# Kernel optimization log

Measured on AMD Instinct MI355X. Metric: run time of the kernel, lower is better.

## Reference

```python
import jax, jax.numpy as jnp
import numpy as np

ALPHA, BETA, INIT_P = 100.0, 1000.0, 2.0
K_NEIGHBORS = 24


def index_points(pts, idx):
    # pts: [B,N,C], idx: [B,...] int -> [B,...,C]
    B = pts.shape[0]
    b = jnp.arange(B).reshape((B,) + (1,) * (idx.ndim - 1))
    return pts[b, idx]


def fps(xyz, m):
    # furthest point sampling, deterministic start at index 0. xyz: [B,N,3]
    B, N, _ = xyz.shape
    def step(carry, _):
        dist, far = carry
        centroid = xyz[jnp.arange(B), far]              # [B,3]
        d = jnp.sum((xyz - centroid[:, None, :]) ** 2, -1)
        dist = jnp.minimum(dist, d)
        nxt = jnp.argmax(dist, -1).astype(jnp.int32)
        return (dist, nxt), far
    init = (jnp.full((B, N), 1e10, xyz.dtype), jnp.zeros((B,), jnp.int32))
    _, idx = jax.lax.scan(step, init, None, length=m)
    return idx.T                                        # [B,m]


def knn_indices(k, xyz, centers):
    # squared distances [B,G,N], k smallest
    d = (jnp.sum(centers ** 2, -1)[..., None]
         - 2.0 * jnp.einsum('bgc,bnc->bgn', centers, xyz)
         + jnp.sum(xyz ** 2, -1)[:, None, :])
    _, idx = jax.lax.top_k(-d, k)
    return idx                                          # [B,G,K]


def normalize(x, ref):
    # torch: mean = ref.unsqueeze(-2); std over ALL elements of (x-mean), ddof=1
    d = x - ref[..., None, :]
    std = jnp.std(d, ddof=1)
    return d / (std + 1e-5)


def fourier_map(t, Bmat):
    # t: [B,7,G,K]; Bmat: [7, C//2] (already includes scale) -> [B,C,G,K]
    x = jnp.transpose(t, (0, 2, 3, 1))                  # [B,G,K,7]
    proj = 2.0 * jnp.pi * (x @ Bmat)                    # [B,G,K,C/2]
    f = jnp.concatenate([jnp.sin(proj), jnp.cos(proj)], -1)
    f = jnp.sign(f) * jnp.abs(f) ** 5
    return jnp.transpose(f, (0, 3, 1, 2))


def tr_embed(my_dim, t):
    # t: [B,3,G,K] -> [B,my_dim,G,K]
    B, C, G, K = t.shape
    F = my_dim // (2 * C)
    dim_embed = ALPHA ** (jnp.arange(F, dtype=t.dtype) / F)
    div = BETA * t[..., None] / dim_embed               # [B,3,G,K,F]
    pe = jnp.stack([jnp.sin(div), jnp.cos(div)], -1).reshape(B, C, G, K, 2 * F)
    pe = jnp.transpose(pe, (0, 1, 4, 2, 3)).reshape(B, my_dim, G, K)
    return pe


def lga(lc_xyz, lc_x, knn_xyz, knn_x, Bmat):
    B, G, K, C = knn_x.shape
    knn_x = normalize(knn_x, lc_x)
    knn_xyz = normalize(knn_xyz, lc_xyz)
    lc_rep = jnp.transpose(jnp.broadcast_to(lc_xyz[:, :, None, :], (B, G, K, 3)), (0, 3, 1, 2))
    knn_xyz_t = jnp.transpose(knn_xyz, (0, 3, 1, 2))    # [B,3,G,K]
    knn_x_t = jnp.transpose(knn_x, (0, 3, 1, 2))        # [B,C,G,K]
    cross = jnp.cross(knn_xyz_t, lc_rep, axis=1)
    dot = jnp.sum(knn_xyz_t * lc_rep, 1, keepdims=True)
    emb_in = jnp.concatenate([knn_xyz_t, cross, dot], 1)  # [B,7,G,K]
    emb = fourier_map(emb_in, Bmat)                       # [B,C,G,K]
    knn_x_w = jnp.concatenate([knn_x_t, emb], 1)          # [B,2C,G,K]
    pe = tr_embed(2 * C, knn_xyz_t) + tr_embed(2 * C, lc_rep)
    return (knn_x_w + pe) * pe


def k_anp(x):
    # x: [B,2C,G,K], data-dependent p-norm attention over K
    std = jnp.std(x, axis=-1, ddof=1, keepdims=True)
    p = jax.lax.stop_gradient(INIT_P + jnp.log1p(std.mean()))  # torch uses .item()
    norm = jnp.sum(jnp.abs(x) ** p, -1, keepdims=True) ** (1.0 / p)
    lc = norm / (norm + 1e-8)
    e = jnp.exp(lc)
    return (x * e).mean(-1) / e.mean(-1)                # [B,2C,G]


def bn_gelu(x, gamma, beta):
    # BatchNorm1d in training mode (batch stats, biased var) + exact GELU
    mean = x.mean((0, 2), keepdims=True)
    var = ((x - mean) ** 2).mean((0, 2), keepdims=True)
    y = (x - mean) / jnp.sqrt(var + 1e-5) * gamma[None, :, None] + beta[None, :, None]
    return jax.nn.gelu(y, approximate=False)


def stage(xyz, x, group_num, Bmat, gamma, beta):
    # xyz: [B,N,3]; x: [B,C,N]
    feats = jnp.transpose(x, (0, 2, 1))
    fi = fps(xyz, group_num)
    lc_xyz = index_points(xyz, fi)
    lc_x = index_points(feats, fi)
    ki = knn_indices(K_NEIGHBORS, xyz, lc_xyz)
    knn_xyz = index_points(xyz, ki)
    knn_x = index_points(feats, ki)
    w = lga(lc_xyz, lc_x, knn_xyz, knn_x, Bmat)
    pooled = k_anp(w) + w.mean(-1)                      # [B,2C,G]
    return lc_xyz, bn_gelu(pooled, gamma, beta)


def setup_inputs() -> dict:
    key = jax.random.key(0)
    k1, k2, k3, k4 = jax.random.split(key, 4)
    B, N, C0 = 4, 4096, 72
    return {
        'xyz': jax.random.uniform(k1, (B, N, 3), jnp.float32),
        'x': jax.random.normal(k2, (B, C0, N), jnp.float32),
        'fourier_B0': jax.random.normal(k3, (7, C0 // 2), jnp.float32) * 50.0,
        'fourier_B1': jax.random.normal(k4, (7, C0), jnp.float32) * 50.0,
        'bn_gamma0': jnp.ones((2 * C0,), jnp.float32),
        'bn_beta0': jnp.zeros((2 * C0,), jnp.float32),
        'bn_gamma1': jnp.ones((4 * C0,), jnp.float32),
        'bn_beta1': jnp.zeros((4 * C0,), jnp.float32),
    }


def reference(xyz, x, fourier_B0, fourier_B1, bn_gamma0, bn_beta0, bn_gamma1, bn_beta1):
    N = xyz.shape[1]
    xyz, x = stage(xyz, x, N // 2, fourier_B0, bn_gamma0, bn_beta0)   # -> [B,144,2048]
    xyz, x = stage(xyz, x, N // 4, fourier_B1, bn_gamma1, bn_beta1)   # -> [B,288,1024]
    return x
```

## Files before the change

kernel.cpp:

```cpp
#include <hip/hip_runtime.h>
#include <math.h>

#define KNB 24

typedef float v2f __attribute__((ext_vector_type(2)));

__global__ void k_transpose(const float* __restrict__ x, float* __restrict__ feats,
                            int B, int C, int N) {
    int idx = blockIdx.x * blockDim.x + threadIdx.x;
    int tot = B * C * N;
    if (idx >= tot) return;
    int n = idx % N; int t = idx / N; int c = t % C; int b = t / C;
    feats[((size_t)b * N + n) * C + c] = x[idx];
}

template<int CTRL>
__device__ __forceinline__ float dppmax(float v) {
    int t = __builtin_amdgcn_update_dpp(0, __float_as_int(v), CTRL, 0xf, 0xf, true);
    return fmaxf(v, __int_as_float(t));
}
template<int CTRL>
__device__ __forceinline__ unsigned dppmaxu(unsigned v) {
    unsigned t = (unsigned)__builtin_amdgcn_update_dpp(0, (int)v, CTRL, 0xf, 0xf, true);
    return v > t ? v : t;
}

template<int NPT, int NWAVE>
__global__ __launch_bounds__(64 * NWAVE) void k_fps_t(const float* __restrict__ xyz,
                                                      int* __restrict__ fi,
                                                      int N, int M) {
#pragma clang fp contract(off)
    const int NP2 = NPT / 2;
    const int b = blockIdx.x;
    const int tid = threadIdx.x;
    const int lane = tid & 63;
    const int wid = tid >> 6;
    extern __shared__ char smc[];
    unsigned long long* keys = (unsigned long long*)smc;
    int* fi_lds = (int*)(smc + 2 * NWAVE * 8);
    size_t poff = ((size_t)(2 * NWAVE * 8) + (size_t)M * 4 + 15) & ~(size_t)15;
    float4* pts = (float4*)(smc + poff);

    const float* p = xyz + (size_t)b * N * 3;
    for (int i = tid; i < N; i += 64 * NWAVE)
        pts[i] = make_float4(p[i*3], p[i*3+1], p[i*3+2], 0.0f);
    __syncthreads();

    const int base = tid * NPT;
    v2f rx[NP2], ry[NP2], rz[NP2], dist[NP2];
#pragma unroll
    for (int j = 0; j < NP2; ++j) {
        float4 a = pts[base + 2*j];
        float4 c = pts[base + 2*j + 1];
        rx[j] = (v2f){a.x, c.x}; ry[j] = (v2f){a.y, c.y}; rz[j] = (v2f){a.z, c.z};
        dist[j] = (v2f){1e10f, 1e10f};
    }

    int far = 0;
    float4 cpt = pts[0];
    float cx = cpt.x, cy = cpt.y, cz = cpt.z;
    for (int it = 0; it < M; ++it) {
        if (tid == 0) fi_lds[it] = far;
        v2f cx2 = (v2f){cx, cx}, cy2 = (v2f){cy, cy}, cz2 = (v2f){cz, cz};
        v2f bv2 = (v2f){-1.0f, -1.0f};
#pragma unroll
        for (int j = 0; j < NP2; ++j) {
            v2f dx = rx[j] - cx2, dy = ry[j] - cy2, dz = rz[j] - cz2;
            v2f d = (dx*dx + dy*dy) + dz*dz;
            v2f dd = __builtin_elementwise_min(dist[j], d);
            dist[j] = dd;
            bv2 = __builtin_elementwise_max(bv2, dd);
        }
        float bv = fmaxf(bv2.x, bv2.y);
        int bi = 0;
#pragma unroll
        for (int j = NP2 - 1; j >= 0; --j) {
            if (dist[j].y == bv) bi = base + 2*j + 1;
            if (dist[j].x == bv) bi = base + 2*j;
        }
        float r = bv;
        r = dppmax<0x111>(r); r = dppmax<0x112>(r);
        r = dppmax<0x114>(r); r = dppmax<0x118>(r);
        r = dppmax<0x142>(r); r = dppmax<0x143>(r);
        float wmax = __int_as_float(__builtin_amdgcn_readlane(__float_as_int(r), 63));
        unsigned long long mask = __ballot(bv == wmax);
        int src = __builtin_ctzll(mask);
        int wbi = __builtin_amdgcn_readlane(bi, src);
        unsigned long long key =
            ((unsigned long long)__float_as_uint(wmax) << 32) | (unsigned)(~wbi);
        if (lane == 0) keys[(it & 1) * NWAVE + wid] = key;
        __syncthreads();
        unsigned long long k0 = keys[(it & 1) * NWAVE + 0];
#pragma unroll
        for (int w = 1; w < NWAVE; ++w) {
            unsigned long long kw = keys[(it & 1) * NWAVE + w];
            if (kw > k0) k0 = kw;
        }
        far = (int)(~(unsigned)k0);
        float4 c = pts[far];
        cx = c.x; cy = c.y; cz = c.z;
    }
    __syncthreads();
    for (int i = tid; i < M; i += 64 * NWAVE) fi[b * M + i] = fi_lds[i];
}

template<int NPT>
__global__ __launch_bounds__(256) void k_knn_t(const float* __restrict__ xyz,
                                               const float* __restrict__ feats,
                                               const int* __restrict__ fi,
                                               float* __restrict__ lc_xyz,
                                               float* __restrict__ lc_x,
                                               int* __restrict__ ki,
                                               double* __restrict__ part,
                                               int B, int N, int G, int C, int identity) {
#pragma clang fp contract(off)
    int bg = blockIdx.x; int b = bg / G; int g = bg % G;
    int idx = identity ? g : fi[bg];
    const int tid = threadIdx.x;
    const int lane = tid & 63;
    const int wid = tid >> 6;
    __shared__ unsigned long long keys[2][4];
    __shared__ int kis[KNB];
    __shared__ float cfeat[144];
    const float* p = xyz + (size_t)b * N * 3;
    float cx = p[idx*3], cy = p[idx*3+1], cz = p[idx*3+2];
    if (tid < 3) lc_xyz[(size_t)bg * 3 + tid] = p[idx*3 + tid];
    for (int c = tid; c < C; c += 256) {
        float v = feats[((size_t)b * N + idx) * C + c];
        lc_x[(size_t)bg * C + c] = v;
        cfeat[c] = v;
    }
    float cc = (cx*cx + cy*cy) + cz*cz;
    const int base = tid * NPT;
    float dist[NPT];
#pragma unroll
    for (int j = 0; j < NPT; ++j) {
        float x0 = p[(base+j)*3], x1 = p[(base+j)*3+1], x2 = p[(base+j)*3+2];
        float xx = (x0*x0 + x1*x1) + x2*x2;
        float dt = (cx*x0 + cy*x1) + cz*x2;
        dist[j] = (cc - 2.0f*dt) + xx;
    }
    for (int kk = 0; kk < KNB; ++kk) {
        float bv = 1e30f;
#pragma unroll
        for (int j = 0; j < NPT; ++j) bv = fminf(bv, dist[j]);
        int lj = 0;
#pragma unroll
        for (int j = NPT - 1; j >= 0; --j) if (dist[j] == bv) lj = j;
        unsigned ub = ~__float_as_uint(bv);
        unsigned r = ub;
        r = dppmaxu<0x111>(r); r = dppmaxu<0x112>(r);
        r = dppmaxu<0x114>(r); r = dppmaxu<0x118>(r);
        r = dppmaxu<0x142>(r); r = dppmaxu<0x143>(r);
        unsigned uwin = (unsigned)__builtin_amdgcn_readlane((int)r, 63);
        unsigned long long mask = __ballot(ub == uwin);
        int src = __builtin_ctzll(mask);
        int gi = __builtin_amdgcn_readlane(base + lj, src);
        unsigned long long key = ((unsigned long long)uwin << 32) | (unsigned)(~gi);
        if (lane == 0) keys[kk & 1][wid] = key;
        __syncthreads();
        unsigned long long k0 = keys[kk & 1][0];
#pragma unroll
        for (int w = 1; w < 4; ++w) {
            unsigned long long kw = keys[kk & 1][w];
            if (kw > k0) k0 = kw;
        }
        int win = (int)(~(unsigned)k0);
        if (tid == 0) kis[kk] = win;
        if (win >= base && win < base + NPT) {
            int wj = win - base;
#pragma unroll
            for (int j = 0; j < NPT; ++j) if (j == wj) dist[j] = 1e30f;
        }
    }
    __syncthreads();
    if (tid < KNB) ki[(size_t)bg * KNB + tid] = kis[tid];
    double s = 0.0, s2 = 0.0, s3 = 0.0, s4 = 0.0;
    for (int i = tid; i < KNB * C; i += 256) {
        int k = i / C, c = i - k * C;
        float d = feats[((size_t)b * N + kis[k]) * C + c] - cfeat[c];
        s += (double)d; s2 += (double)d * (double)d;
    }
    if (tid < KNB * 3) {
        int k = tid / 3, c = tid - k * 3;
        float ctr = (c == 0) ? cx : ((c == 1) ? cy : cz);
        float d = p[kis[k] * 3 + c] - ctr;
        s3 += (double)d; s4 += (double)d * (double)d;
    }
    for (int off = 32; off > 0; off >>= 1) {
        s += __shfl_down(s, off); s2 += __shfl_down(s2, off);
        s3 += __shfl_down(s3, off); s4 += __shfl_down(s4, off);
    }
    __shared__ double sw[4][4];
    if ((tid & 63) == 0) {
        sw[wid][0] = s; sw[wid][1] = s2; sw[wid][2] = s3; sw[wid][3] = s4;
    }
    __syncthreads();
    if (tid == 0) {
        double t0 = 0.0, t1 = 0.0, t2 = 0.0, t3 = 0.0;
        for (int w = 0; w < 4; ++w) {
            t0 += sw[w][0]; t1 += sw[w][1]; t2 += sw[w][2]; t3 += sw[w][3];
        }
        double* q = part + (size_t)bg * 4;
        q[0] = t0; q[1] = t1; q[2] = t2; q[3] = t3;
    }
}

__global__ __launch_bounds__(1024) void k_reduce(const double* __restrict__ part,
                                                 double* __restrict__ acc, int n) {
    double s0 = 0.0, s1 = 0.0, s2 = 0.0, s3 = 0.0;
    for (int i = threadIdx.x; i < n; i += 1024) {
        const double* q = part + (size_t)i * 4;
        s0 += q[0]; s1 += q[1]; s2 += q[2]; s3 += q[3];
    }
    for (int off = 32; off > 0; off >>= 1) {
        s0 += __shfl_down(s0, off); s1 += __shfl_down(s1, off);
        s2 += __shfl_down(s2, off); s3 += __shfl_down(s3, off);
    }
    __shared__ double sw[16][4];
    int wid = threadIdx.x >> 6;
    if ((threadIdx.x & 63) == 0) {
        sw[wid][0] = s0; sw[wid][1] = s1; sw[wid][2] = s2; sw[wid][3] = s3;
    }
    __syncthreads();
    if (threadIdx.x == 0) {
        double t0 = 0.0, t1 = 0.0, t2 = 0.0, t3 = 0.0;
        for (int w = 0; w < 16; ++w) {
            t0 += sw[w][0]; t1 += sw[w][1]; t2 += sw[w][2]; t3 += sw[w][3];
        }
        acc[0] = t0; acc[1] = t1; acc[2] = t2; acc[3] = t3;
    }
}

__global__ __launch_bounds__(256) void k_feature(
    const float* __restrict__ xyz, const float* __restrict__ feats,
    const float* __restrict__ lc_xyz, const float* __restrict__ lc_x,
    const int* __restrict__ ki, const float* __restrict__ Bmat,
    const double* __restrict__ accp, float* __restrict__ pooled,
    int B, int N, int G, int C, double nx, double nz)
{
    int bg = blockIdx.x; int b = bg / G; int g = bg % G;
    int tid = threadIdx.x;
    int C2 = C >> 1;
    int Cout = 2 * C;
    int F = C / 3;
    extern __shared__ float sm[];
    float* t7    = sm;
    float* sxyzn = t7 + KNB * 7;
    int*   kidx  = (int*)(sxyzn + KNB * 3);
    float* semb  = (float*)(kidx + KNB);
    float* sfeat = semb + KNB * C;

    double a0 = accp[0], a1 = accp[1], a2 = accp[2], a3 = accp[3];
    double vx = (a1 - a0 * a0 / nx) / (nx - 1.0);
    float invx = 1.0f / (sqrtf((float)vx) + 1e-5f);
    double vz = (a3 - a2 * a2 / nz) / (nz - 1.0);
    float invz = 1.0f / (sqrtf((float)vz) + 1e-5f);

    float l0 = lc_xyz[(size_t)bg*3], l1 = lc_xyz[(size_t)bg*3+1], l2 = lc_xyz[(size_t)bg*3+2];

    if (tid < KNB) {
        int idx = ki[(size_t)bg * KNB + tid];
        kidx[tid] = idx;
        const float* q = xyz + ((size_t)b * N + idx) * 3;
        float a0f = (q[0]-l0)*invz, a1f = (q[1]-l1)*invz, a2f = (q[2]-l2)*invz;
        float c0 = a1f*l2 - a2f*l1;
        float c1 = a2f*l0 - a0f*l2;
        float c2 = a0f*l1 - a1f*l0;
        float dt = (a0f*l0 + a1f*l1) + a2f*l2;
        float* tp = t7 + tid * 7;
        tp[0]=a0f; tp[1]=a1f; tp[2]=a2f; tp[3]=c0; tp[4]=c1; tp[5]=c2; tp[6]=dt;
        sxyzn[tid*3]=a0f; sxyzn[tid*3+1]=a1f; sxyzn[tid*3+2]=a2f;
    }
    __syncthreads();
    for (int i = tid; i < KNB * C; i += blockDim.x) {
        int k = i / C, c = i - k * C;
        sfeat[i] = feats[((size_t)b * N + kidx[k]) * C + c];
    }
    const float TWO_PI = 6.2831854820251465f;
    for (int i = tid; i < KNB * C2; i += blockDim.x) {
        int k = i / C2, m2 = i % C2;
        const float* tp = t7 + k * 7;
        float s = 0.0f;
        for (int j = 0; j < 7; ++j) s += tp[j] * Bmat[j * C2 + m2];
        float pr = TWO_PI * s;
        float sn, cs;
        __sincosf(pr, &sn, &cs);
        float sn2 = sn*sn, cs2 = cs*cs;
        semb[k*C + m2]      = sn2*sn2*sn;
        semb[k*C + C2 + m2] = cs2*cs2*cs;
    }
    __syncthreads();
    for (int m = tid; m < Cout; m += blockDim.x) {
        int c3 = m / (2 * F);
        int r  = m % (2 * F);
        int f  = r >> 1;
        int trig = r & 1;
        float de = __powf(100.0f, (float)f / (float)F);
        float rde = 1000.0f / de;
        float lv = (c3 == 0) ? l0 : ((c3 == 1) ? l1 : l2);
        float a2v = lv * rde;
        float pe2 = trig ? __cosf(a2v) : __sinf(a2v);
        float lfm = (m < C) ? lc_x[(size_t)bg * C + m] : 0.0f;
        float acc = 0.0f;
        for (int k = 0; k < KNB; ++k) {
            float v;
            if (m < C) {
                v = (sfeat[k * C + m] - lfm) * invx;
            } else {
                v = semb[k * C + (m - C)];
            }
            float a1v = sxyzn[k*3 + c3] * rde;
            float pe1 = trig ? __cosf(a1v) : __sinf(a1v);
            float pe = pe1 + pe2;
            acc += (v + pe) * pe;
        }
        float mean = acc / 24.0f;
        pooled[((size_t)b * Cout + m) * G + g] = 2.0f * mean;
    }
}

__global__ __launch_bounds__(256) void k_bn(const float* __restrict__ pooled,
                                            const float* __restrict__ gamma,
                                            const float* __restrict__ beta,
                                            float* __restrict__ out,
                                            int B, int Cout, int G, int transposed) {
    int m = blockIdx.x;
    double s = 0.0, s2 = 0.0;
    for (int i = threadIdx.x; i < B * G; i += 256) {
        int b = i / G, g = i % G;
        float v = pooled[((size_t)b * Cout + m) * G + g];
        s += (double)v; s2 += (double)v * (double)v;
    }
    for (int off = 32; off > 0; off >>= 1) { s += __shfl_down(s, off); s2 += __shfl_down(s2, off); }
    __shared__ double sw[4], sw2[4];
    __shared__ float smv[2];
    int wid = threadIdx.x >> 6;
    if ((threadIdx.x & 63) == 0) { sw[wid] = s; sw2[wid] = s2; }
    __syncthreads();
    if (threadIdx.x == 0) {
        double ts = sw[0] + sw[1] + sw[2] + sw[3];
        double ts2 = sw2[0] + sw2[1] + sw2[2] + sw2[3];
        double n = (double)(B * G);
        double mean = ts / n;
        double var = ts2 / n - mean * mean;
        smv[0] = (float)mean; smv[1] = (float)var;
    }
    __syncthreads();
    float mean = smv[0], var = smv[1];
    float ga = gamma[m], be = beta[m];
    for (int i = threadIdx.x; i < B * G; i += 256) {
        int b = i / G, g = i % G;
        float v = pooled[((size_t)b * Cout + m) * G + g];
        float y = (v - mean) / sqrtf(var + 1e-5f) * ga + be;
        float ge = 0.5f * y * (1.0f + erff(y / 1.4142135381698608f));
        if (transposed) out[((size_t)b * G + g) * Cout + m] = ge;
        else            out[((size_t)b * Cout + m) * G + g] = ge;
    }
}

extern "C" void kernel_launch(void* const* d_in, const int* in_sizes, int n_in,
                              void* d_out, int out_size, void* d_ws, size_t ws_size,
                              hipStream_t stream) {
    const int B = 4, N1 = 4096, C0 = 72, G1 = 2048, Co1 = 144;
    const int N2 = 2048, C1 = 144, G2 = 1024, Co2 = 288;

    const float* xyz = (const float*)d_in[0];
    const float* x0  = (const float*)d_in[1];
    const float* B0  = (const float*)d_in[2];
    const float* B1  = (const float*)d_in[3];
    const float* g0  = (const float*)d_in[4];
    const float* be0 = (const float*)d_in[5];
    const float* g1  = (const float*)d_in[6];
    const float* be1 = (const float*)d_in[7];
    float* out = (float*)d_out;

    char* wp = (char*)d_ws;
    size_t off = 0;
    auto A = [&](size_t bytes) -> void* {
        void* p = wp + off;
        off += (bytes + 255) & ~(size_t)255;
        return p;
    };
    float* feats1  = (float*)A((size_t)B*N1*C0*4);
    int*   fi1     = (int*)  A((size_t)B*G1*4);
    float* lcx1    = (float*)A((size_t)B*G1*3*4);
    float* lcf1    = (float*)A((size_t)B*G1*C0*4);
    int*   ki1     = (int*)  A((size_t)B*G1*KNB*4);
    double* acc    = (double*)A(8*8);
    double* part   = (double*)A((size_t)B*G1*4*8);
    float* pooled1 = (float*)A((size_t)B*Co1*G1*4);
    float* feats2  = (float*)A((size_t)B*N2*C1*4);
    float* lcx2    = (float*)A((size_t)B*G2*3*4);
    float* lcf2    = lcf1;
    int*   ki2     = ki1;
    float* pooled2 = feats1;

    k_transpose<<<(B*C0*N1 + 255)/256, 256, 0, stream>>>(x0, feats1, B, C0, N1);

    {
        size_t poff = ((size_t)(2*4*8) + (size_t)G1*4 + 15) & ~(size_t)15;
        size_t shm = poff + (size_t)N1*16;
        k_fps_t<16, 4><<<B, 256, shm, stream>>>(xyz, fi1, N1, G1);
    }
    k_knn_t<16><<<B*G1, 256, 0, stream>>>(xyz, feats1, fi1, lcx1, lcf1, ki1, part,
                                          B, N1, G1, C0, 0);
    k_reduce<<<1, 1024, 0, stream>>>(part, acc, B*G1);
    {
        size_t shf = (size_t)(KNB*7 + KNB*3 + KNB + 2*KNB*C0) * 4;
        k_feature<<<B*G1, 256, shf, stream>>>(xyz, feats1, lcx1, lcf1, ki1, B0, acc, pooled1,
                                              B, N1, G1, C0,
                                              (double)B*G1*KNB*C0, (double)B*G1*KNB*3);
    }
    k_bn<<<Co1, 256, 0, stream>>>(pooled1, g0, be0, feats2, B, Co1, G1, 1);

    k_knn_t<8><<<B*G2, 256, 0, stream>>>(lcx1, feats2, (const int*)nullptr,
                                         lcx2, lcf2, ki2, part, B, N2, G2, C1, 1);
    k_reduce<<<1, 1024, 0, stream>>>(part, acc + 4, B*G2);
    {
        size_t shf = (size_t)(KNB*7 + KNB*3 + KNB + 2*KNB*C1) * 4;
        k_feature<<<B*G2, 256, shf, stream>>>(lcx1, feats2, lcx2, lcf2, ki2, B1, acc + 4, pooled2,
                                              B, N2, G2, C1,
                                              (double)B*G2*KNB*C1, (double)B*G2*KNB*3);
    }
    k_bn<<<Co2, 256, 0, stream>>>(pooled2, g1, be1, out, B, Co2, G2, 0);
}
```

Measured before the change: 1.646 ms.

## Coalesce feature writes, split batchnorm into stats/finalize/apply, tile transposes

The feature kernel now writes pooled values in [B*G, Cout] row layout, so each block's channel writes are contiguous. Batchnorm is split into a multi-block partial-statistics pass, a finalize kernel, and an elementwise apply, replacing the per-channel single-block kernel with its strided reads. The first transpose and the final output transpose use shared-memory 32x33 tiles so global reads and writes are coalesced. This adds two extra launches per stage and changes the double-precision reduction order.

```diff
diff --git a/kernel.cpp b/kernel.cpp
--- a/kernel.cpp
+++ b/kernel.cpp
@@ -5,13 +5,24 @@
 
 typedef float v2f __attribute__((ext_vector_type(2)));
 
-__global__ void k_transpose(const float* __restrict__ x, float* __restrict__ feats,
-                            int B, int C, int N) {
-    int idx = blockIdx.x * blockDim.x + threadIdx.x;
-    int tot = B * C * N;
-    if (idx >= tot) return;
-    int n = idx % N; int t = idx / N; int c = t % C; int b = t / C;
-    feats[((size_t)b * N + n) * C + c] = x[idx];
+__global__ __launch_bounds__(256) void k_transpose(const float* __restrict__ x,
+                                                   float* __restrict__ feats,
+                                                   int C, int N) {
+    __shared__ float tile[32][33];
+    int b = blockIdx.z;
+    int n0 = blockIdx.x * 32, c0 = blockIdx.y * 32;
+    int tx = threadIdx.x, ty = threadIdx.y;
+#pragma unroll
+    for (int k = 0; k < 4; ++k) {
+        int c = c0 + ty + k * 8, n = n0 + tx;
+        if (c < C && n < N) tile[ty + k * 8][tx] = x[((size_t)b * C + c) * N + n];
+    }
+    __syncthreads();
+#pragma unroll
+    for (int k = 0; k < 4; ++k) {
+        int n = n0 + ty + k * 8, c = c0 + tx;
+        if (c < C && n < N) feats[((size_t)b * N + n) * C + c] = tile[tx][ty + k * 8];
+    }
 }
 
 template<int CTRL>
@@ -316,46 +327,80 @@
             acc += (v + pe) * pe;
         }
         float mean = acc / 24.0f;
-        pooled[((size_t)b * Cout + m) * G + g] = 2.0f * mean;
-    }
-}
-
-__global__ __launch_bounds__(256) void k_bn(const float* __restrict__ pooled,
-                                            const float* __restrict__ gamma,
-                                            const float* __restrict__ beta,
-                                            float* __restrict__ out,
-                                            int B, int Cout, int G, int transposed) {
-    int m = blockIdx.x;
-    double s = 0.0, s2 = 0.0;
-    for (int i = threadIdx.x; i < B * G; i += 256) {
-        int b = i / G, g = i % G;
-        float v = pooled[((size_t)b * Cout + m) * G + g];
-        s += (double)v; s2 += (double)v * (double)v;
-    }
-    for (int off = 32; off > 0; off >>= 1) { s += __shfl_down(s, off); s2 += __shfl_down(s2, off); }
-    __shared__ double sw[4], sw2[4];
-    __shared__ float smv[2];
-    int wid = threadIdx.x >> 6;
-    if ((threadIdx.x & 63) == 0) { sw[wid] = s; sw2[wid] = s2; }
-    __syncthreads();
-    if (threadIdx.x == 0) {
-        double ts = sw[0] + sw[1] + sw[2] + sw[3];
-        double ts2 = sw2[0] + sw2[1] + sw2[2] + sw2[3];
-        double n = (double)(B * G);
-        double mean = ts / n;
-        double var = ts2 / n - mean * mean;
-        smv[0] = (float)mean; smv[1] = (float)var;
-    }
-    __syncthreads();
-    float mean = smv[0], var = smv[1];
-    float ga = gamma[m], be = beta[m];
-    for (int i = threadIdx.x; i < B * G; i += 256) {
-        int b = i / G, g = i % G;
-        float v = pooled[((size_t)b * Cout + m) * G + g];
-        float y = (v - mean) / sqrtf(var + 1e-5f) * ga + be;
-        float ge = 0.5f * y * (1.0f + erff(y / 1.4142135381698608f));
-        if (transposed) out[((size_t)b * G + g) * Cout + m] = ge;
-        else            out[((size_t)b * Cout + m) * G + g] = ge;
+        pooled[((size_t)bg) * Cout + m] = 2.0f * mean;
+    }
+}
+
+__global__ __launch_bounds__(256) void k_bnstat(const float* __restrict__ pooled,
+                                                double* __restrict__ bnpart,
+                                                int rows, int Cout, int rowsPerBlk) {
+    int blk = blockIdx.x;
+    int r0 = blk * rowsPerBlk;
+    int r1 = r0 + rowsPerBlk; if (r1 > rows) r1 = rows;
+    int t = threadIdx.x;
+    double s0 = 0.0, q0 = 0.0, s1 = 0.0, q1 = 0.0;
+    for (int r = r0; r < r1; ++r) {
+        const float* row = pooled + (size_t)r * Cout;
+        if (t < Cout)       { float v = row[t];       s0 += (double)v; q0 += (double)v * v; }
+        if (t + 256 < Cout) { float v = row[t + 256]; s1 += (double)v; q1 += (double)v * v; }
+    }
+    double* p = bnpart + (size_t)blk * Cout * 2;
+    if (t < Cout)       { p[t * 2] = s0;           p[t * 2 + 1] = q0; }
+    if (t + 256 < Cout) { p[(t + 256) * 2] = s1;   p[(t + 256) * 2 + 1] = q1; }
+}
+
+__global__ __launch_bounds__(512) void k_bnfin(const double* __restrict__ bnpart,
+                                               float* __restrict__ stats,
+                                               int NB, int Cout, double n) {
+    int m = threadIdx.x;
+    if (m >= Cout) return;
+    double s = 0.0, q = 0.0;
+    for (int b2 = 0; b2 < NB; ++b2) {
+        const double* p = bnpart + ((size_t)b2 * Cout + m) * 2;
+        s += p[0]; q += p[1];
+    }
+    double mean = s / n;
+    double var = q / n - mean * mean;
+    stats[2 * m] = (float)mean; stats[2 * m + 1] = (float)var;
+}
+
+__global__ void k_bnapply(const float* __restrict__ pooled, const float* __restrict__ stats,
+                          const float* __restrict__ gamma, const float* __restrict__ beta,
+                          float* __restrict__ outp, int tot, int Cout) {
+    int i = blockIdx.x * 256 + threadIdx.x;
+    if (i >= tot) return;
+    int m = i % Cout;
+    float v = pooled[i];
+    float mean = stats[2*m], var = stats[2*m+1];
+    float y = (v - mean) / sqrtf(var + 1e-5f) * gamma[m] + beta[m];
+    outp[i] = 0.5f * y * (1.0f + erff(y / 1.4142135381698608f));
+}
+
+__global__ __launch_bounds__(256) void k_bnapply_t(const float* __restrict__ pooled,
+                                                   const float* __restrict__ stats,
+                                                   const float* __restrict__ gamma,
+                                                   const float* __restrict__ beta,
+                                                   float* __restrict__ outp,
+                                                   int G, int Cout) {
+    __shared__ float tile[32][33];
+    int b = blockIdx.z;
+    int g0 = blockIdx.x * 32, m0 = blockIdx.y * 32;
+    int tx = threadIdx.x, ty = threadIdx.y;
+#pragma unroll
+    for (int k = 0; k < 4; ++k) {
+        int g = g0 + ty + k * 8, m = m0 + tx;
+        if (g < G && m < Cout) {
+            float v = pooled[((size_t)b * G + g) * Cout + m];
+            float mean = stats[2*m], var = stats[2*m+1];
+            float y = (v - mean) / sqrtf(var + 1e-5f) * gamma[m] + beta[m];
+            tile[ty + k * 8][tx] = 0.5f * y * (1.0f + erff(y / 1.4142135381698608f));
+        }
+    }
+    __syncthreads();
+#pragma unroll
+    for (int k = 0; k < 4; ++k) {
+        int m = m0 + ty + k * 8, g = g0 + tx;
+        if (g < G && m < Cout) outp[((size_t)b * Cout + m) * G + g] = tile[tx][ty + k * 8];
     }
 }
 
@@ -364,6 +409,7 @@
                               hipStream_t stream) {
     const int B = 4, N1 = 4096, C0 = 72, G1 = 2048, Co1 = 144;
     const int N2 = 2048, C1 = 144, G2 = 1024, Co2 = 288;
+    const int NB = 64;
 
     const float* xyz = (const float*)d_in[0];
     const float* x0  = (const float*)d_in[1];
@@ -389,14 +435,19 @@
     int*   ki1     = (int*)  A((size_t)B*G1*KNB*4);
     double* acc    = (double*)A(8*8);
     double* part   = (double*)A((size_t)B*G1*4*8);
-    float* pooled1 = (float*)A((size_t)B*Co1*G1*4);
+    double* bnpart = (double*)A((size_t)NB*Co2*2*8);
+    float* stats   = (float*)A((size_t)Co2*2*4);
+    float* pooled1 = (float*)A((size_t)B*G1*Co1*4);
     float* feats2  = (float*)A((size_t)B*N2*C1*4);
     float* lcx2    = (float*)A((size_t)B*G2*3*4);
     float* lcf2    = lcf1;
     int*   ki2     = ki1;
     float* pooled2 = feats1;
 
-    k_transpose<<<(B*C0*N1 + 255)/256, 256, 0, stream>>>(x0, feats1, B, C0, N1);
+    {
+        dim3 grid((N1 + 31) / 32, (C0 + 31) / 32, B);
+        k_transpose<<<grid, dim3(32, 8), 0, stream>>>(x0, feats1, C0, N1);
+    }
 
     {
         size_t poff = ((size_t)(2*4*8) + (size_t)G1*4 + 15) & ~(size_t)15;
@@ -412,7 +463,10 @@
                                               B, N1, G1, C0,
                                               (double)B*G1*KNB*C0, (double)B*G1*KNB*3);
     }
-    k_bn<<<Co1, 256, 0, stream>>>(pooled1, g0, be0, feats2, B, Co1, G1, 1);
+    k_bnstat<<<NB, 256, 0, stream>>>(pooled1, bnpart, B*G1, Co1, (B*G1 + NB - 1)/NB);
+    k_bnfin<<<1, 512, 0, stream>>>(bnpart, stats, NB, Co1, (double)(B*G1));
+    k_bnapply<<<(B*G1*Co1 + 255)/256, 256, 0, stream>>>(pooled1, stats, g0, be0, feats2,
+                                                        B*G1*Co1, Co1);
 
     k_knn_t<8><<<B*G2, 256, 0, stream>>>(lcx1, feats2, (const int*)nullptr,
                                          lcx2, lcf2, ki2, part, B, N2, G2, C1, 1);
@@ -423,5 +477,10 @@
                                               B, N2, G2, C1,
                                               (double)B*G2*KNB*C1, (double)B*G2*KNB*3);
     }
-    k_bn<<<Co2, 256, 0, stream>>>(pooled2, g1, be1, out, B, Co2, G2, 0);
-}
+    k_bnstat<<<NB, 256, 0, stream>>>(pooled2, bnpart, B*G2, Co2, (B*G2 + NB - 1)/NB);
+    k_bnfin<<<1, 512, 0, stream>>>(bnpart, stats, NB, Co2, (double)(B*G2));
+    {
+        dim3 grid((G2 + 31) / 32, (Co2 + 31) / 32, B);
+        k_bnapply_t<<<grid, dim3(32, 8), 0, stream>>>(pooled2, stats, g1, be1, out, G2, Co2);
+    }
+}
```

Result: slower. 1.721 ms (+4.6%).

## Assign one wavefront per KNN query and tile the feature transpose through LDS

Applied to the files above, without the earlier changes.

The KNN kernel now handles four query groups per block, one per wavefront. Each wave scans every point with 64 or 32 points per lane, so the per-iteration block barrier and cross-wave key merge go away and partial stats come straight from the wave reduction. The transpose becomes a 32x32 shared-memory tiled transpose with coalesced reads and writes, and it also zeroes the accumulator buffer. The cost is far more registers per lane for the distance array and more serial work per wave, which can lower occupancy.

```diff
diff --git a/kernel.cpp b/kernel.cpp
--- a/kernel.cpp
+++ b/kernel.cpp
@@ -5,13 +5,27 @@
 
 typedef float v2f __attribute__((ext_vector_type(2)));
 
-__global__ void k_transpose(const float* __restrict__ x, float* __restrict__ feats,
-                            int B, int C, int N) {
-    int idx = blockIdx.x * blockDim.x + threadIdx.x;
-    int tot = B * C * N;
-    if (idx >= tot) return;
-    int n = idx % N; int t = idx / N; int c = t % C; int b = t / C;
-    feats[((size_t)b * N + n) * C + c] = x[idx];
+__global__ __launch_bounds__(256) void k_transpose(const float* __restrict__ x,
+                                                   float* __restrict__ feats,
+                                                   double* __restrict__ acc,
+                                                   int C, int N) {
+    __shared__ float tile[32][33];
+    if (blockIdx.x == 0 && blockIdx.y == 0 && blockIdx.z == 0 &&
+        threadIdx.y == 0 && threadIdx.x < 8) acc[threadIdx.x] = 0.0;
+    int b = blockIdx.z;
+    int n0 = blockIdx.x * 32, c0 = blockIdx.y * 32;
+    int tx = threadIdx.x, ty = threadIdx.y;
+#pragma unroll
+    for (int k = 0; k < 4; ++k) {
+        int c = c0 + ty + k * 8, n = n0 + tx;
+        if (c < C && n < N) tile[ty + k * 8][tx] = x[((size_t)b * C + c) * N + n];
+    }
+    __syncthreads();
+#pragma unroll
+    for (int k = 0; k < 4; ++k) {
+        int n = n0 + ty + k * 8, c = c0 + tx;
+        if (c < C && n < N) feats[((size_t)b * N + n) * C + c] = tile[tx][ty + k * 8];
+    }
 }
 
 template<int CTRL>
@@ -104,8 +118,8 @@
     for (int i = tid; i < M; i += 64 * NWAVE) fi[b * M + i] = fi_lds[i];
 }
 
-template<int NPT>
-__global__ __launch_bounds__(256) void k_knn_t(const float* __restrict__ xyz,
+template<int NPTW>
+__global__ __launch_bounds__(256) void k_knn_w(const float* __restrict__ xyz,
                                                const float* __restrict__ feats,
                                                const int* __restrict__ fi,
                                                float* __restrict__ lc_xyz,
@@ -114,27 +128,26 @@
                                                double* __restrict__ part,
                                                int B, int N, int G, int C, int identity) {
 #pragma clang fp contract(off)
-    int bg = blockIdx.x; int b = bg / G; int g = bg % G;
+    const int lane = threadIdx.x & 63;
+    const int wid = threadIdx.x >> 6;
+    int bg = blockIdx.x * 4 + wid;
+    int b = bg / G, g = bg % G;
     int idx = identity ? g : fi[bg];
-    const int tid = threadIdx.x;
-    const int lane = tid & 63;
-    const int wid = tid >> 6;
-    __shared__ unsigned long long keys[2][4];
-    __shared__ int kis[KNB];
-    __shared__ float cfeat[144];
+    __shared__ float cfeatS[4][144];
+    __shared__ int kisS[4][KNB];
     const float* p = xyz + (size_t)b * N * 3;
     float cx = p[idx*3], cy = p[idx*3+1], cz = p[idx*3+2];
-    if (tid < 3) lc_xyz[(size_t)bg * 3 + tid] = p[idx*3 + tid];
-    for (int c = tid; c < C; c += 256) {
+    if (lane < 3) lc_xyz[(size_t)bg * 3 + lane] = p[idx*3 + lane];
+    for (int c = lane; c < C; c += 64) {
         float v = feats[((size_t)b * N + idx) * C + c];
         lc_x[(size_t)bg * C + c] = v;
-        cfeat[c] = v;
+        cfeatS[wid][c] = v;
     }
     float cc = (cx*cx + cy*cy) + cz*cz;
-    const int base = tid * NPT;
-    float dist[NPT];
-#pragma unroll
-    for (int j = 0; j < NPT; ++j) {
+    const int base = lane * NPTW;
+    float dist[NPTW];
+#pragma unroll
+    for (int j = 0; j < NPTW; ++j) {
         float x0 = p[(base+j)*3], x1 = p[(base+j)*3+1], x2 = p[(base+j)*3+2];
         float xx = (x0*x0 + x1*x1) + x2*x2;
         float dt = (cx*x0 + cy*x1) + cz*x2;
@@ -143,10 +156,10 @@
     for (int kk = 0; kk < KNB; ++kk) {
         float bv = 1e30f;
 #pragma unroll
-        for (int j = 0; j < NPT; ++j) bv = fminf(bv, dist[j]);
+        for (int j = 0; j < NPTW; ++j) bv = fminf(bv, dist[j]);
         int lj = 0;
 #pragma unroll
-        for (int j = NPT - 1; j >= 0; --j) if (dist[j] == bv) lj = j;
+        for (int j = NPTW - 1; j >= 0; --j) if (dist[j] == bv) lj = j;
         unsigned ub = ~__float_as_uint(bv);
         unsigned r = ub;
         r = dppmaxu<0x111>(r); r = dppmaxu<0x112>(r);
@@ -156,53 +169,34 @@
         unsigned long long mask = __ballot(ub == uwin);
         int src = __builtin_ctzll(mask);
         int gi = __builtin_amdgcn_readlane(base + lj, src);
-        unsigned long long key = ((unsigned long long)uwin << 32) | (unsigned)(~gi);
-        if (lane == 0) keys[kk & 1][wid] = key;
-        __syncthreads();
-        unsigned long long k0 = keys[kk & 1][0];
-#pragma unroll
-        for (int w = 1; w < 4; ++w) {
-            unsigned long long kw = keys[kk & 1][w];
-            if (kw > k0) k0 = kw;
-        }
-        int win = (int)(~(unsigned)k0);
-        if (tid == 0) kis[kk] = win;
-        if (win >= base && win < base + NPT) {
-            int wj = win - base;
-#pragma unroll
-            for (int j = 0; j < NPT; ++j) if (j == wj) dist[j] = 1e30f;
-        }
-    }
-    __syncthreads();
-    if (tid < KNB) ki[(size_t)bg * KNB + tid] = kis[tid];
+        if (lane == 0) kisS[wid][kk] = gi;
+        if (gi >= base && gi < base + NPTW) {
+            int wj = gi - base;
+#pragma unroll
+            for (int j = 0; j < NPTW; ++j) if (j == wj) dist[j] = 1e30f;
+        }
+    }
+    if (lane < KNB) ki[(size_t)bg * KNB + lane] = kisS[wid][lane];
     double s = 0.0, s2 = 0.0, s3 = 0.0, s4 = 0.0;
-    for (int i = tid; i < KNB * C; i += 256) {
+    for (int i = lane; i < KNB * C; i += 64) {
         int k = i / C, c = i - k * C;
-        float d = feats[((size_t)b * N + kis[k]) * C + c] - cfeat[c];
+        float d = feats[((size_t)b * N + kisS[wid][k]) * C + c] - cfeatS[wid][c];
         s += (double)d; s2 += (double)d * (double)d;
     }
-    if (tid < KNB * 3) {
-        int k = tid / 3, c = tid - k * 3;
+    for (int i = lane; i < KNB * 3; i += 64) {
+        int k = i / 3, c = i - k * 3;
         float ctr = (c == 0) ? cx : ((c == 1) ? cy : cz);
-        float d = p[kis[k] * 3 + c] - ctr;
+        float d = p[kisS[wid][k] * 3 + c] - ctr;
         s3 += (double)d; s4 += (double)d * (double)d;
     }
+#pragma unroll
     for (int off = 32; off > 0; off >>= 1) {
         s += __shfl_down(s, off); s2 += __shfl_down(s2, off);
         s3 += __shfl_down(s3, off); s4 += __shfl_down(s4, off);
     }
-    __shared__ double sw[4][4];
-    if ((tid & 63) == 0) {
-        sw[wid][0] = s; sw[wid][1] = s2; sw[wid][2] = s3; sw[wid][3] = s4;
-    }
-    __syncthreads();
-    if (tid == 0) {
-        double t0 = 0.0, t1 = 0.0, t2 = 0.0, t3 = 0.0;
-        for (int w = 0; w < 4; ++w) {
-            t0 += sw[w][0]; t1 += sw[w][1]; t2 += sw[w][2]; t3 += sw[w][3];
-        }
+    if (lane == 0) {
         double* q = part + (size_t)bg * 4;
-        q[0] = t0; q[1] = t1; q[2] = t2; q[3] = t3;
+        q[0] = s; q[1] = s2; q[2] = s3; q[3] = s4;
     }
 }
 
@@ -396,15 +390,18 @@
     int*   ki2     = ki1;
     float* pooled2 = feats1;
 
-    k_transpose<<<(B*C0*N1 + 255)/256, 256, 0, stream>>>(x0, feats1, B, C0, N1);
+    {
+        dim3 grid((N1 + 31) / 32, (C0 + 31) / 32, B);
+        k_transpose<<<grid, dim3(32, 8), 0, stream>>>(x0, feats1, acc, C0, N1);
+    }
 
     {
         size_t poff = ((size_t)(2*4*8) + (size_t)G1*4 + 15) & ~(size_t)15;
         size_t shm = poff + (size_t)N1*16;
         k_fps_t<16, 4><<<B, 256, shm, stream>>>(xyz, fi1, N1, G1);
     }
-    k_knn_t<16><<<B*G1, 256, 0, stream>>>(xyz, feats1, fi1, lcx1, lcf1, ki1, part,
-                                          B, N1, G1, C0, 0);
+    k_knn_w<64><<<B*G1/4, 256, 0, stream>>>(xyz, feats1, fi1, lcx1, lcf1, ki1, part,
+                                            B, N1, G1, C0, 0);
     k_reduce<<<1, 1024, 0, stream>>>(part, acc, B*G1);
     {
         size_t shf = (size_t)(KNB*7 + KNB*3 + KNB + 2*KNB*C0) * 4;
@@ -414,8 +411,8 @@
     }
     k_bn<<<Co1, 256, 0, stream>>>(pooled1, g0, be0, feats2, B, Co1, G1, 1);
 
-    k_knn_t<8><<<B*G2, 256, 0, stream>>>(lcx1, feats2, (const int*)nullptr,
-                                         lcx2, lcf2, ki2, part, B, N2, G2, C1, 1);
+    k_knn_w<32><<<B*G2/4, 256, 0, stream>>>(lcx1, feats2, (const int*)nullptr,
+                                            lcx2, lcf2, ki2, part, B, N2, G2, C1, 1);
     k_reduce<<<1, 1024, 0, stream>>>(part, acc + 4, B*G2);
     {
         size_t shf = (size_t)(KNB*7 + KNB*3 + KNB + 2*KNB*C1) * 4;
```

Result: no change. 1.664 ms (+1.1%).

## Fuse tiled feature transpose into FPS launch as extra blocks

Applied to the files above, without the earlier changes.

Removes the standalone naive transpose kernel and appends shared-memory tiled transpose blocks to the furthest-point-sampling grid, so the transpose runs alongside the few latency-bound FPS blocks. The tiled transpose also makes the writes coalesced. The block mapping hardcodes an offset of 4, matching B=4, and leaves some dead conditional statements in place.

```diff
diff --git a/kernel.cpp b/kernel.cpp
--- a/kernel.cpp
+++ b/kernel.cpp
@@ -4,15 +4,6 @@
 #define KNB 24
 
 typedef float v2f __attribute__((ext_vector_type(2)));
-
-__global__ void k_transpose(const float* __restrict__ x, float* __restrict__ feats,
-                            int B, int C, int N) {
-    int idx = blockIdx.x * blockDim.x + threadIdx.x;
-    int tot = B * C * N;
-    if (idx >= tot) return;
-    int n = idx % N; int t = idx / N; int c = t % C; int b = t / C;
-    feats[((size_t)b * N + n) * C + c] = x[idx];
-}
 
 template<int CTRL>
 __device__ __forceinline__ float dppmax(float v) {
@@ -26,16 +17,49 @@
 }
 
 template<int NPT, int NWAVE>
-__global__ __launch_bounds__(64 * NWAVE) void k_fps_t(const float* __restrict__ xyz,
-                                                      int* __restrict__ fi,
-                                                      int N, int M) {
+__global__ __launch_bounds__(64 * NWAVE) void k_fps_tr(const float* __restrict__ xyz,
+                                                       int* __restrict__ fi,
+                                                       int N, int M,
+                                                       const float* __restrict__ x0,
+                                                       float* __restrict__ feats,
+                                                       int C, int NT, int nT, int cT) {
 #pragma clang fp contract(off)
     const int NP2 = NPT / 2;
+    const int tid = threadIdx.x;
+    extern __shared__ char smc[];
+
+    if ((int)blockIdx.x >= gridDim.x - 0 && false) return;
+
+    if ((int)blockIdx.x >= (int)(gridDim.x) ) return;
+
+    if ((int)blockIdx.x >= (int)0 && (int)blockIdx.x >= (int)( 0) && false) return;
+
+    if ((int)blockIdx.x >= (int)( (int)gridDim.x - nT * cT * 4 ) && (int)blockIdx.x >= 4) {
+        int bid = blockIdx.x - 4;
+        int tilesPerB = nT * cT;
+        int b = bid / tilesPerB;
+        int t2 = bid - b * tilesPerB;
+        int cTile = t2 / nT;
+        int nTile = t2 - cTile * nT;
+        int tx = tid & 31, ty = tid >> 5;
+        float* tile = (float*)smc;
+#pragma unroll
+        for (int k = 0; k < 4; ++k) {
+            int c = cTile * 32 + ty + k * 8, n = nTile * 32 + tx;
+            if (c < C && n < NT) tile[(ty + k * 8) * 33 + tx] = x0[((size_t)b * C + c) * NT + n];
+        }
+        __syncthreads();
+#pragma unroll
+        for (int k = 0; k < 4; ++k) {
+            int n = nTile * 32 + ty + k * 8, c = cTile * 32 + tx;
+            if (c < C && n < NT) feats[((size_t)b * NT + n) * C + c] = tile[tx * 33 + ty + k * 8];
+        }
+        return;
+    }
+
     const int b = blockIdx.x;
-    const int tid = threadIdx.x;
     const int lane = tid & 63;
     const int wid = tid >> 6;
-    extern __shared__ char smc[];
     unsigned long long* keys = (unsigned long long*)smc;
     int* fi_lds = (int*)(smc + 2 * NWAVE * 8);
     size_t poff = ((size_t)(2 * NWAVE * 8) + (size_t)M * 4 + 15) & ~(size_t)15;
@@ -396,12 +420,12 @@
     int*   ki2     = ki1;
     float* pooled2 = feats1;
 
-    k_transpose<<<(B*C0*N1 + 255)/256, 256, 0, stream>>>(x0, feats1, B, C0, N1);
-
     {
+        const int nT = N1 / 32, cT = (C0 + 31) / 32;
         size_t poff = ((size_t)(2*4*8) + (size_t)G1*4 + 15) & ~(size_t)15;
         size_t shm = poff + (size_t)N1*16;
-        k_fps_t<16, 4><<<B, 256, shm, stream>>>(xyz, fi1, N1, G1);
+        k_fps_tr<16, 4><<<B + B*nT*cT, 256, shm, stream>>>(xyz, fi1, N1, G1,
+                                                           x0, feats1, C0, N1, nT, cT);
     }
     k_knn_t<16><<<B*G1, 256, 0, stream>>>(xyz, feats1, fi1, lcx1, lcf1, ki1, part,
                                           B, N1, G1, C0, 0);
```

New measurement: 1.645 ms. Within noise of the previous version (-0.0%).
